# Performance work log

Measured on AMD Instinct MI355X. Metric: run time of the kernel, lower is better.

The kernel has to match this reference:

```python
import jax, jax.numpy as jnp
import numpy as np

B, C, H, W = 8, 192, 128, 128
E, HID, TOP_K = 4, 384, 2


def setup_inputs() -> dict:
    key = jax.random.key(0)
    ks = jax.random.split(key, 5)
    sn = lambda k, sh, sc: jax.random.normal(k, sh, jnp.float32) * sc
    return {
        "x": jax.random.normal(ks[0], (B, C, H, W), jnp.float32),
        "router_w": sn(ks[1], (E, C), C ** -0.5),
        "router_b": jnp.zeros((E,), jnp.float32),
        "fc1_w": sn(ks[2], (E, HID, C), C ** -0.5),
        "fc1_b": jnp.zeros((E, HID), jnp.float32),
        "fc2_w": sn(ks[3], (E, C, HID), HID ** -0.5),
        "fc2_b": jnp.zeros((E, C), jnp.float32),
        "scale": jnp.array([0.1], jnp.float32),
    }


def reference(x, router_w, router_b, fc1_w, fc1_b, fc2_w, fc2_b, scale):
    b, c, h, w = x.shape
    e = router_w.shape[0]
    # (B,C,H,W) -> (B, N, C) tokens
    tokens = jnp.transpose(x, (0, 2, 3, 1)).reshape(b, h * w, c)
    logits = tokens @ router_w.T + router_b            # (B,N,E)
    topv, topi = jax.lax.top_k(logits, TOP_K)          # (B,N,K)
    wts = jax.nn.softmax(topv, axis=-1)                # (B,N,K)
    # per-expert combine weight: sum_k wts_k * [topi_k == e]  -> (B,N,E)
    gates = jnp.sum(jax.nn.one_hot(topi, e, dtype=tokens.dtype) * wts[..., None], axis=-2)
    out = jnp.zeros_like(tokens)
    for ei in range(e):  # small fixed expert count
        hid = jax.nn.gelu(tokens @ fc1_w[ei].T + fc1_b[ei], approximate=False)
        y_e = hid @ fc2_w[ei].T + fc2_b[ei]
        out = out + gates[..., ei:ei + 1] * y_e
    out = jnp.transpose(out.reshape(b, h, w, c), (0, 3, 1, 2))
    return x + scale[0] * out
```

## Files before the change

### kernel.cpp

```cpp
#include <hip/hip_runtime.h>
#include <stdint.h>

typedef __attribute__((ext_vector_type(4))) float f32x4;
typedef unsigned long long u64;
typedef __attribute__((ext_vector_type(2))) u64 u64x2;

#define CC   192
#define NN   16384
#define EE   4
#define HIDD 384

#define OFF_H0   12800u
#define OFF_H1   25600u
#define OFF_PART 12800
#define OFF_GATE 38400
#define LDS_SZ   39424
#define ROWS     200u

__device__ __forceinline__ uint32_t fp8b(float f){
  uint32_t u = __builtin_bit_cast(uint32_t, f);
  uint32_t s = (u >> 24) & 0x80u;
  float af = fminf(__builtin_fabsf(f), 448.0f);
  if (af < 0.015625f) return s;
  uint32_t v = __builtin_bit_cast(uint32_t, af);
  v += 0x7FFFFu + ((v >> 20) & 1u);
  uint32_t e = (v >> 23) - 120u;
  return s | (e << 3) | ((v >> 20) & 7u);
}
#if __has_builtin(__builtin_amdgcn_cvt_pk_fp8_f32)
__device__ __forceinline__ uint32_t fp8x4(float a, float b, float c, float d){
  int v = __builtin_amdgcn_cvt_pk_fp8_f32(a, b, 0, false);
  v = __builtin_amdgcn_cvt_pk_fp8_f32(c, d, v, true);
  return (uint32_t)v;
}
#else
__device__ __forceinline__ uint32_t fp8x4(float a, float b, float c, float d){
  return fp8b(a) | (fp8b(b) << 8) | (fp8b(c) << 16) | (fp8b(d) << 24);
}
#endif
__device__ __forceinline__ float gelu_f(float v){
  float e = __builtin_amdgcn_exp2f(v * -2.4554669f);
  return v * __builtin_amdgcn_rcpf(1.0f + e);
}
__device__ __forceinline__ f32x4 mfma8(u64 a, u64 b, f32x4 c){
  asm("v_mfma_f32_16x16x32_fp8_fp8 %0, %1, %2, %0" : "+v"(c) : "v"(a), "v"(b));
  return c;
}

#define WAITV(n) do{ asm volatile("s_waitcnt vmcnt(" #n ")"); \
                     __builtin_amdgcn_sched_barrier(0); }while(0)
#define BARRIER() do{ __builtin_amdgcn_sched_barrier(0); \
                      asm volatile("s_waitcnt lgkmcnt(0)"); \
                      __builtin_amdgcn_s_barrier(); \
                      __builtin_amdgcn_sched_barrier(0); }while(0)

__device__ __forceinline__ void issue_w1(const uint8_t* a0, const uint8_t* a1,
                                         const uint8_t* a2, const float* bb,
                                         u64x2 (&w)[9], f32x4 (&bv)[3]){
  asm volatile(
    "global_load_dwordx4 %0, %[A0], off\n\t"
    "global_load_dwordx4 %1, %[A0], off offset:16\n\t"
    "global_load_dwordx4 %2, %[A0], off offset:32\n\t"
    "global_load_dwordx4 %3, %[A1], off\n\t"
    "global_load_dwordx4 %4, %[A1], off offset:16\n\t"
    "global_load_dwordx4 %5, %[A1], off offset:32\n\t"
    "global_load_dwordx4 %6, %[A2], off\n\t"
    "global_load_dwordx4 %7, %[A2], off offset:16\n\t"
    "global_load_dwordx4 %8, %[A2], off offset:32\n\t"
    "global_load_dwordx4 %9, %[B], off\n\t"
    "global_load_dwordx4 %10, %[B], off offset:64\n\t"
    "global_load_dwordx4 %11, %[B], off offset:128"
    : "=&v"(w[0]), "=&v"(w[1]), "=&v"(w[2]), "=&v"(w[3]), "=&v"(w[4]), "=&v"(w[5]),
      "=&v"(w[6]), "=&v"(w[7]), "=&v"(w[8]), "=&v"(bv[0]), "=&v"(bv[1]), "=&v"(bv[2])
    : [A0]"v"(a0), [A1]"v"(a1), [A2]"v"(a2), [B]"v"(bb));
}
__device__ __forceinline__ void issue_w2(const uint8_t* a0, const uint8_t* a1,
                                         const uint8_t* a2, u64x2 (&w)[9]){
  asm volatile(
    "global_load_dwordx4 %0, %[A0], off\n\t"
    "global_load_dwordx4 %1, %[A0], off offset:16\n\t"
    "global_load_dwordx4 %2, %[A0], off offset:32\n\t"
    "global_load_dwordx4 %3, %[A1], off\n\t"
    "global_load_dwordx4 %4, %[A1], off offset:16\n\t"
    "global_load_dwordx4 %5, %[A1], off offset:32\n\t"
    "global_load_dwordx4 %6, %[A2], off\n\t"
    "global_load_dwordx4 %7, %[A2], off offset:16\n\t"
    "global_load_dwordx4 %8, %[A2], off offset:32"
    : "=&v"(w[0]), "=&v"(w[1]), "=&v"(w[2]), "=&v"(w[3]), "=&v"(w[4]), "=&v"(w[5]),
      "=&v"(w[6]), "=&v"(w[7]), "=&v"(w[8])
    : [A0]"v"(a0), [A1]"v"(a1), [A2]"v"(a2));
}

extern "C" __global__ void kconv(const float* __restrict__ w1, const float* __restrict__ w2,
                                 uint8_t* __restrict__ w1f8, uint8_t* __restrict__ w2f8){
  int i = blockIdx.x * 256 + threadIdx.x;
  {
    int row = i / 192, k = i % 192;
    int o = k >> 3, kk = o >> 2, lg = o & 3, bi = k & 7;
    w1f8[(size_t)row * 192 + lg * 48 + kk * 8 + bi] = (uint8_t)fp8b(w1[i]);
  }
  {
    int row = i / 384, k = i % 384;
    int o = k >> 3, kk = o >> 2, lg = o & 3, bi = k & 7;
    w2f8[(size_t)row * 384 + lg * 96 + kk * 8 + bi] = (uint8_t)fp8b(w2[i]);
  }
}

__global__ __launch_bounds__(256)
__attribute__((amdgpu_waves_per_eu(2, 2)))
void kmoe(const float* __restrict__ x, const float* __restrict__ rw,
          const float* __restrict__ rb, const uint8_t* __restrict__ w1f8,
          const float* __restrict__ b1, const uint8_t* __restrict__ w2f8,
          const float* __restrict__ b2, const float* __restrict__ scp,
          float* __restrict__ out)
{
  __shared__ __align__(16) unsigned char S[LDS_SZ];
  const int tid  = threadIdx.x;
  const int lane = tid & 63;
  const int wv   = tid >> 6;
  const int lq   = lane & 15;
  const int lg   = lane >> 4;
  const int tile = blockIdx.x;
  const int b    = tile >> 8;
  const int n0   = (tile & 255) << 6;
  const float* xb = x + (size_t)b * CC * NN;

  {
    const int t = lane;
    const uint32_t rowbase = (uint32_t)t * ROWS;
    float a0 = 0.f, a1 = 0.f, a2 = 0.f, a3 = 0.f;
    #pragma unroll
    for (int jj = 0; jj < 6; ++jj){
      float v[8];
      #pragma unroll
      for (int j = 0; j < 8; ++j){
        const int c = wv * 48 + jj * 8 + j;
        v[j] = xb[(size_t)c * NN + n0 + t];
        a0 = __builtin_fmaf(v[j], rw[c],          a0);
        a1 = __builtin_fmaf(v[j], rw[CC + c],     a1);
        a2 = __builtin_fmaf(v[j], rw[2 * CC + c], a2);
        a3 = __builtin_fmaf(v[j], rw[3 * CC + c], a3);
      }
      uint2 p;
      p.x = fp8x4(v[0], v[1], v[2], v[3]);
      p.y = fp8x4(v[4], v[5], v[6], v[7]);
      *(uint2*)(S + rowbase + (uint32_t)(wv * 48 + jj * 8)) = p;
    }
    float* pl = (float*)(S + OFF_PART);
    pl[(wv * 4 + 0) * 64 + t] = a0;
    pl[(wv * 4 + 1) * 64 + t] = a1;
    pl[(wv * 4 + 2) * 64 + t] = a2;
    pl[(wv * 4 + 3) * 64 + t] = a3;
  }
  __syncthreads();

  if (tid < 64){
    const int t = tid;
    const float* pl = (const float*)(S + OFF_PART);
    float l0 = rb[0], l1 = rb[1], l2 = rb[2], l3 = rb[3];
    #pragma unroll
    for (int cg = 0; cg < 4; ++cg){
      l0 += pl[(cg * 4 + 0) * 64 + t];
      l1 += pl[(cg * 4 + 1) * 64 + t];
      l2 += pl[(cg * 4 + 2) * 64 + t];
      l3 += pl[(cg * 4 + 3) * 64 + t];
    }
    int i1 = 0; float v1 = l0;
    if (l1 > v1){ v1 = l1; i1 = 1; }
    if (l2 > v1){ v1 = l2; i1 = 2; }
    if (l3 > v1){ v1 = l3; i1 = 3; }
    float v2 = -3.0e38f; int i2 = 0;
    if (i1 != 0){ v2 = l0; i2 = 0; }
    if (i1 != 1 && l1 > v2){ v2 = l1; i2 = 1; }
    if (i1 != 2 && l2 > v2){ v2 = l2; i2 = 2; }
    if (i1 != 3 && l3 > v2){ v2 = l3; i2 = 3; }
    const float ex = __expf(v2 - v1);
    const float ga = 1.0f / (1.0f + ex);
    const float gb = ex * ga;
    float* glw = (float*)(S + OFF_GATE);
    glw[t * 4 + 0] = (i1 == 0) ? ga : ((i2 == 0) ? gb : 0.0f);
    glw[t * 4 + 1] = (i1 == 1) ? ga : ((i2 == 1) ? gb : 0.0f);
    glw[t * 4 + 2] = (i1 == 2) ? ga : ((i2 == 2) ? gb : 0.0f);
    glw[t * 4 + 3] = (i1 == 3) ? ga : ((i2 == 3) ? gb : 0.0f);
  }
  __syncthreads();

  const float* gl = (const float*)(S + OFF_GATE);
  uint32_t rowb[4];
  #pragma unroll
  for (int np = 0; np < 4; ++np) rowb[np] = (uint32_t)(16 * np + lq) * ROWS;

  const uint8_t* w1l = w1f8 + (size_t)(wv * 48 + lq) * 192 + lg * 48;
  const uint8_t* w2l = w2f8 + (size_t)(wv * 48 + lq) * 384 + lg * 96;
  const float*   b1l = b1 + wv * 48 + 4 * lg;

  u64x2 W1[9], W2[9];
  f32x4 BV[3];
  f32x4 oacc[3][4];
  #pragma unroll
  for (int m = 0; m < 3; ++m)
    #pragma unroll
    for (int np = 0; np < 4; ++np)
      oacc[m][np] = (f32x4){0.f, 0.f, 0.f, 0.f};

#define ISSUE_W1(p) issue_w1(w1l + (size_t)(p) * 36864, \
                             w1l + (size_t)(p) * 36864 + 16 * 192, \
                             w1l + (size_t)(p) * 36864 + 32 * 192, \
                             b1l + (p) * 192, W1, BV)
#define ISSUE_W2(e, ch) issue_w2(w2l + (size_t)(e) * 73728 + (ch) * 48, \
                                 w2l + (size_t)(e) * 73728 + (ch) * 48 + 16 * 384, \
                                 w2l + (size_t)(e) * 73728 + (ch) * 48 + 32 * 384, W2)

#define G1_COMP(hacc) do{ \
    _Pragma("unroll") \
    for (int m = 0; m < 3; ++m) \
      _Pragma("unroll") \
      for (int np = 0; np < 4; ++np) hacc[m][np] = BV[m]; \
    __builtin_amdgcn_s_setprio(1); \
    _Pragma("unroll") \
    for (int kk = 0; kk < 6; ++kk){ \
      u64 xk[4]; \
      _Pragma("unroll") \
      for (int np = 0; np < 4; ++np) \
        xk[np] = *(const u64*)(S + rowb[np] + (uint32_t)(kk * 32 + lg * 8)); \
      _Pragma("unroll") \
      for (int np = 0; np < 4; ++np) \
        _Pragma("unroll") \
        for (int m = 0; m < 3; ++m){ \
          const u64 a = (kk & 1) ? W1[m * 3 + (kk >> 1)].y : W1[m * 3 + (kk >> 1)].x; \
          hacc[m][np] = mfma8(a, xk[np], hacc[m][np]); \
        } \
    } \
    __builtin_amdgcn_s_setprio(0); }while(0)

#define G2_COMP(hb) do{ \
    __builtin_amdgcn_s_setprio(1); \
    _Pragma("unroll") \
    for (int kk = 0; kk < 6; ++kk){ \
      u64 hf[4]; \
      _Pragma("unroll") \
      for (int np = 0; np < 4; ++np) \
        hf[np] = *(const u64*)(S + (hb) + rowb[np] + (uint32_t)(kk * 32 + lg * 8)); \
      _Pragma("unroll") \
      for (int np = 0; np < 4; ++np) \
        _Pragma("unroll") \
        for (int m = 0; m < 3; ++m){ \
          const u64 a = (kk & 1) ? W2[m * 3 + (kk >> 1)].y : W2[m * 3 + (kk >> 1)].x; \
          oacc[m][np] = mfma8(a, hf[np], oacc[m][np]); \
        } \
    } \
    __builtin_amdgcn_s_setprio(0); }while(0)

#define GELU_ST(hb, e, hacc) do{ \
    _Pragma("unroll") \
    for (int np = 0; np < 4; ++np){ \
      const float g = gl[(16 * np + lq) * 4 + (e)]; \
      _Pragma("unroll") \
      for (int m = 0; m < 3; ++m){ \
        const uint32_t colb = (uint32_t)(48 * wv + 16 * m + 4 * lg); \
        *(uint32_t*)(S + (hb) + rowb[np] + colb) = \
          fp8x4(gelu_f(hacc[m][np][0]) * g, gelu_f(hacc[m][np][1]) * g, \
                gelu_f(hacc[m][np][2]) * g, gelu_f(hacc[m][np][3]) * g); \
      } \
    } }while(0)

  {
    ISSUE_W1(0);
    ISSUE_W2(0, 0);
    WAITV(9);
    f32x4 hacc[3][4];
    G1_COMP(hacc);
    GELU_ST(OFF_H0, 0, hacc);
    ISSUE_W1(1);
  }
  BARRIER();

  #pragma unroll 1
  for (int i = 0; i < 7; ++i){
    const uint32_t hb_r = (i & 1) ? OFF_H1 : OFF_H0;
    const uint32_t hb_w = (i & 1) ? OFF_H0 : OFF_H1;
    WAITV(12);
    G2_COMP(hb_r);
    {
      const int p = i + 1;
      ISSUE_W2(p >> 1, p & 1);
    }
    WAITV(9);
    f32x4 hacc[3][4];
    G1_COMP(hacc);
    GELU_ST(hb_w, (i + 1) >> 1, hacc);
    if (i < 6) ISSUE_W1(i + 2);
    BARRIER();
  }

  WAITV(0);
  G2_COMP(OFF_H1);

  {
    const float sc = scp[0];
    f32x4 g4v[4];
    #pragma unroll
    for (int np = 0; np < 4; ++np)
      g4v[np] = *(const f32x4*)(S + OFF_GATE + (16 * np + lq) * 16);
    const size_t obase = (size_t)b * CC * NN + n0;
    #pragma unroll
    for (int m = 0; m < 3; ++m){
      const int f0 = 48 * wv + 16 * m + 4 * lg;
      f32x4 b2q[4];
      #pragma unroll
      for (int e = 0; e < 4; ++e)
        b2q[e] = *(const f32x4*)(b2 + e * CC + f0);
      #pragma unroll
      for (int np = 0; np < 4; ++np){
        const int tok = 16 * np + lq;
        #pragma unroll
        for (int r = 0; r < 4; ++r){
          const float bt = __builtin_fmaf(g4v[np][0], b2q[0][r],
                            __builtin_fmaf(g4v[np][1], b2q[1][r],
                             __builtin_fmaf(g4v[np][2], b2q[2][r],
                                            g4v[np][3] * b2q[3][r])));
          const size_t off = obase + (size_t)(f0 + r) * NN + tok;
          out[off] = __builtin_fmaf(sc, oacc[m][np][r] + bt, x[off]);
        }
      }
    }
  }
#undef ISSUE_W1
#undef ISSUE_W2
#undef G1_COMP
#undef G2_COMP
#undef GELU_ST
}

extern "C" void kernel_launch(void* const* d_in, const int* in_sizes, int n_in,
                              void* d_out, int out_size, void* d_ws, size_t ws_size,
                              hipStream_t stream){
  const float* x  = (const float*)d_in[0];
  const float* rw = (const float*)d_in[1];
  const float* rb = (const float*)d_in[2];
  const float* w1 = (const float*)d_in[3];
  const float* b1 = (const float*)d_in[4];
  const float* w2 = (const float*)d_in[5];
  const float* b2 = (const float*)d_in[6];
  const float* sc = (const float*)d_in[7];
  float* out = (float*)d_out;
  uint8_t* w1f8 = (uint8_t*)d_ws;
  uint8_t* w2f8 = w1f8 + 294912;

  hipLaunchKernelGGL(kconv, dim3(1152), dim3(256), 0, stream, w1, w2, w1f8, w2f8);
  hipLaunchKernelGGL(kmoe,  dim3(2048), dim3(256), 0, stream,
                     x, rw, rb, w1f8, b1, w2f8, b2, sc, out);
}
```

Baseline: 166.3 us.

## Route tokens per expert via LDS lists to skip unselected token-expert pairs

Builds per-expert token lists in LDS with ballot/popcount after the router, so each expert's FC1/FC2 MFMA work runs only over groups of 16 tokens that actually selected it. This replaces the dense compute of all four experts for every token. Partial outputs are scattered into a new fp32 LDS accumulation buffer, and the final epilogue reads from it to do the coalesced residual write. In exchange, LDS use roughly doubles, which can lower occupancy, and the change adds extra barriers, gather indirection and LDS read-modify-write traffic.

```diff
diff --git a/kernel.cpp b/kernel.cpp
--- a/kernel.cpp
+++ b/kernel.cpp
@@ -10,12 +10,16 @@
 #define EE   4
 #define HIDD 384
 
-#define OFF_H0   12800u
-#define OFF_H1   25600u
-#define OFF_PART 12800
-#define OFF_GATE 38400
-#define LDS_SZ   39424
-#define ROWS     200u
+#define OFF_X    0u
+#define OFF_HID  12800u
+#define OFF_PART 12800u
+#define OFF_OUT  25600u
+#define OFF_GATE 76560u
+#define OFF_LIST 77584u
+#define OFF_CNT  78608u
+#define LDS_SZ   78640
+#define XROWB    200u
+#define OROWB    784u
 
 __device__ __forceinline__ uint32_t fp8b(float f){
   uint32_t u = __builtin_bit_cast(uint32_t, f);
@@ -127,7 +131,7 @@
 
   {
     const int t = lane;
-    const uint32_t rowbase = (uint32_t)t * ROWS;
+    const uint32_t rowbase = (uint32_t)t * XROWB;
     float a0 = 0.f, a1 = 0.f, a2 = 0.f, a3 = 0.f;
     #pragma unroll
     for (int jj = 0; jj < 6; ++jj){
@@ -182,13 +186,30 @@
     glw[t * 4 + 1] = (i1 == 1) ? ga : ((i2 == 1) ? gb : 0.0f);
     glw[t * 4 + 2] = (i1 == 2) ? ga : ((i2 == 2) ? gb : 0.0f);
     glw[t * 4 + 3] = (i1 == 3) ? ga : ((i2 == 3) ? gb : 0.0f);
+    uint32_t* lst = (uint32_t*)(S + OFF_LIST);
+    uint32_t* cw  = (uint32_t*)(S + OFF_CNT);
+    #pragma unroll
+    for (int e = 0; e < 4; ++e){
+      const bool mine = (i1 == e) || (i2 == e);
+      const u64 msk = __ballot(mine);
+      const int cnt = __popcll(msk);
+      const int ng  = (cnt + 15) >> 4;
+      if (mine){
+        const int slot = (int)__popcll(msk & ((1ull << t) - 1ull));
+        lst[e * 64 + slot] = (uint32_t)t;
+      }
+      if (t >= cnt && t < ng * 16) lst[e * 64 + t] = 0u;
+      if (t == 0){ cw[e] = (uint32_t)ng; cw[4 + e] = (uint32_t)cnt; }
+    }
   }
   __syncthreads();
 
   const float* gl = (const float*)(S + OFF_GATE);
-  uint32_t rowb[4];
+  const uint32_t* lst = (const uint32_t*)(S + OFF_LIST);
+  const int* cw = (const int*)(S + OFF_CNT);
+  uint32_t rowh[4];
   #pragma unroll
-  for (int np = 0; np < 4; ++np) rowb[np] = (uint32_t)(16 * np + lq) * ROWS;
+  for (int np = 0; np < 4; ++np) rowh[np] = OFF_HID + (uint32_t)(16 * np + lq) * XROWB;
 
   const uint8_t* w1l = w1f8 + (size_t)(wv * 48 + lq) * 192 + lg * 48;
   const uint8_t* w2l = w2f8 + (size_t)(wv * 48 + lq) * 384 + lg * 96;
@@ -210,126 +231,173 @@
 #define ISSUE_W2(e, ch) issue_w2(w2l + (size_t)(e) * 73728 + (ch) * 48, \
                                  w2l + (size_t)(e) * 73728 + (ch) * 48 + 16 * 384, \
                                  w2l + (size_t)(e) * 73728 + (ch) * 48 + 32 * 384, W2)
-
-#define G1_COMP(hacc) do{ \
+#define LOAD_TOK(tk, e) do{ \
+    _Pragma("unroll") \
+    for (int np = 0; np < 4; ++np) tk[np] = lst[(e) * 64 + np * 16 + lq]; }while(0)
+
+#define G1_NP(np, tk, hacc) do{ \
+    const uint32_t xrow = OFF_X + tk[np] * XROWB; \
+    _Pragma("unroll") \
+    for (int kk = 0; kk < 6; ++kk){ \
+      const u64 xk = *(const u64*)(S + xrow + (uint32_t)(kk * 32 + lg * 8)); \
+      _Pragma("unroll") \
+      for (int m = 0; m < 3; ++m){ \
+        const u64 a = (kk & 1) ? W1[m * 3 + (kk >> 1)].y : W1[m * 3 + (kk >> 1)].x; \
+        hacc[m][np] = mfma8(a, xk, hacc[m][np]); \
+      } \
+    } }while(0)
+#define G1_COMP(ng, tk, hacc) do{ \
     _Pragma("unroll") \
     for (int m = 0; m < 3; ++m) \
       _Pragma("unroll") \
       for (int np = 0; np < 4; ++np) hacc[m][np] = BV[m]; \
     __builtin_amdgcn_s_setprio(1); \
+    if (0 < (ng)) G1_NP(0, tk, hacc); \
+    if (1 < (ng)) G1_NP(1, tk, hacc); \
+    if (2 < (ng)) G1_NP(2, tk, hacc); \
+    if (3 < (ng)) G1_NP(3, tk, hacc); \
+    __builtin_amdgcn_s_setprio(0); }while(0)
+
+#define G2_NP(np) do{ \
     _Pragma("unroll") \
     for (int kk = 0; kk < 6; ++kk){ \
-      u64 xk[4]; \
+      const u64 hf = *(const u64*)(S + rowh[np] + (uint32_t)(kk * 32 + lg * 8)); \
       _Pragma("unroll") \
-      for (int np = 0; np < 4; ++np) \
-        xk[np] = *(const u64*)(S + rowb[np] + (uint32_t)(kk * 32 + lg * 8)); \
-      _Pragma("unroll") \
-      for (int np = 0; np < 4; ++np) \
+      for (int m = 0; m < 3; ++m){ \
+        const u64 a = (kk & 1) ? W2[m * 3 + (kk >> 1)].y : W2[m * 3 + (kk >> 1)].x; \
+        oacc[m][np] = mfma8(a, hf, oacc[m][np]); \
+      } \
+    } }while(0)
+#define G2_COMP(ng) do{ \
+    __builtin_amdgcn_s_setprio(1); \
+    if (0 < (ng)) G2_NP(0); \
+    if (1 < (ng)) G2_NP(1); \
+    if (2 < (ng)) G2_NP(2); \
+    if (3 < (ng)) G2_NP(3); \
+    __builtin_amdgcn_s_setprio(0); }while(0)
+
+#define GELU_ST(e, ng, ct, tk, hacc) do{ \
+    _Pragma("unroll") \
+    for (int np = 0; np < 4; ++np){ \
+      if (np < (ng)){ \
+        const float g = (np * 16 + lq < (ct)) ? gl[tk[np] * 4 + (e)] : 0.0f; \
         _Pragma("unroll") \
         for (int m = 0; m < 3; ++m){ \
-          const u64 a = (kk & 1) ? W1[m * 3 + (kk >> 1)].y : W1[m * 3 + (kk >> 1)].x; \
-          hacc[m][np] = mfma8(a, xk[np], hacc[m][np]); \
+          *(uint32_t*)(S + rowh[np] + (uint32_t)(48 * wv + 16 * m + 4 * lg)) = \
+            fp8x4(gelu_f(hacc[m][np][0]) * g, gelu_f(hacc[m][np][1]) * g, \
+                  gelu_f(hacc[m][np][2]) * g, gelu_f(hacc[m][np][3]) * g); \
         } \
-    } \
-    __builtin_amdgcn_s_setprio(0); }while(0)
-
-#define G2_COMP(hb) do{ \
-    __builtin_amdgcn_s_setprio(1); \
-    _Pragma("unroll") \
-    for (int kk = 0; kk < 6; ++kk){ \
-      u64 hf[4]; \
-      _Pragma("unroll") \
-      for (int np = 0; np < 4; ++np) \
-        hf[np] = *(const u64*)(S + (hb) + rowb[np] + (uint32_t)(kk * 32 + lg * 8)); \
-      _Pragma("unroll") \
-      for (int np = 0; np < 4; ++np) \
+      } \
+    } }while(0)
+
+#define SCATTER(e, ng, ct, tk) do{ \
+    _Pragma("unroll") \
+    for (int np = 0; np < 4; ++np){ \
+      if (np < (ng)){ \
+        const uint32_t srow = (np * 16 + lq < (ct)) ? tk[np] : 64u; \
         _Pragma("unroll") \
         for (int m = 0; m < 3; ++m){ \
-          const u64 a = (kk & 1) ? W2[m * 3 + (kk >> 1)].y : W2[m * 3 + (kk >> 1)].x; \
-          oacc[m][np] = mfma8(a, hf[np], oacc[m][np]); \
+          float* p = (float*)(S + OFF_OUT + srow * OROWB \
+                              + (uint32_t)((48 * wv + 16 * m + 4 * lg) * 4)); \
+          f32x4 c = *(const f32x4*)p; \
+          c += oacc[m][np]; \
+          *(f32x4*)p = c; \
         } \
-    } \
-    __builtin_amdgcn_s_setprio(0); }while(0)
-
-#define GELU_ST(hb, e, hacc) do{ \
-    _Pragma("unroll") \
-    for (int np = 0; np < 4; ++np){ \
-      const float g = gl[(16 * np + lq) * 4 + (e)]; \
+      } \
       _Pragma("unroll") \
-      for (int m = 0; m < 3; ++m){ \
-        const uint32_t colb = (uint32_t)(48 * wv + 16 * m + 4 * lg); \
-        *(uint32_t*)(S + (hb) + rowb[np] + colb) = \
-          fp8x4(gelu_f(hacc[m][np][0]) * g, gelu_f(hacc[m][np][1]) * g, \
-                gelu_f(hacc[m][np][2]) * g, gelu_f(hacc[m][np][3]) * g); \
-      } \
+      for (int m = 0; m < 3; ++m) oacc[m][np] = (f32x4){0.f, 0.f, 0.f, 0.f}; \
     } }while(0)
 
-  {
-    ISSUE_W1(0);
-    ISSUE_W2(0, 0);
+  ISSUE_W1(0);
+  ISSUE_W2(0, 0);
+  {
+    f32x4* oz = (f32x4*)(S + OFF_OUT);
+    for (int i = tid; i < 65 * 49; i += 256) oz[i] = (f32x4){0.f, 0.f, 0.f, 0.f};
+  }
+  {
+    const int ng = __builtin_amdgcn_readfirstlane(cw[0]);
+    const int ct = __builtin_amdgcn_readfirstlane(cw[4]);
+    uint32_t tk[4];
+    LOAD_TOK(tk, 0);
     WAITV(9);
     f32x4 hacc[3][4];
-    G1_COMP(hacc);
-    GELU_ST(OFF_H0, 0, hacc);
+    G1_COMP(ng, tk, hacc);
+    GELU_ST(0, ng, ct, tk, hacc);
     ISSUE_W1(1);
   }
   BARRIER();
 
   #pragma unroll 1
   for (int i = 0; i < 7; ++i){
-    const uint32_t hb_r = (i & 1) ? OFF_H1 : OFF_H0;
-    const uint32_t hb_w = (i & 1) ? OFF_H0 : OFF_H1;
+    const int e2 = i >> 1;
+    const int p1 = i + 1, e1 = p1 >> 1, ch1 = p1 & 1;
     WAITV(12);
-    G2_COMP(hb_r);
     {
-      const int p = i + 1;
-      ISSUE_W2(p >> 1, p & 1);
-    }
+      const int ng2 = __builtin_amdgcn_readfirstlane(cw[e2]);
+      G2_COMP(ng2);
+      if (i & 1){
+        const int ct2 = __builtin_amdgcn_readfirstlane(cw[4 + e2]);
+        uint32_t tk2[4];
+        LOAD_TOK(tk2, e2);
+        SCATTER(e2, ng2, ct2, tk2);
+      }
+    }
+    ISSUE_W2(e1, ch1);
     WAITV(9);
-    f32x4 hacc[3][4];
-    G1_COMP(hacc);
-    GELU_ST(hb_w, (i + 1) >> 1, hacc);
+    {
+      const int ng1 = __builtin_amdgcn_readfirstlane(cw[e1]);
+      const int ct1 = __builtin_amdgcn_readfirstlane(cw[4 + e1]);
+      uint32_t tk1[4];
+      LOAD_TOK(tk1, e1);
+      f32x4 hacc[3][4];
+      G1_COMP(ng1, tk1, hacc);
+      BARRIER();
+      GELU_ST(e1, ng1, ct1, tk1, hacc);
+    }
     if (i < 6) ISSUE_W1(i + 2);
     BARRIER();
   }
 
   WAITV(0);
-  G2_COMP(OFF_H1);
-
-  {
+  {
+    const int ng = __builtin_amdgcn_readfirstlane(cw[3]);
+    const int ct = __builtin_amdgcn_readfirstlane(cw[4 + 3]);
+    G2_COMP(ng);
+    uint32_t tk[4];
+    LOAD_TOK(tk, 3);
+    SCATTER(3, ng, ct, tk);
+  }
+  BARRIER();
+
+  {
+    const int t = lane;
     const float sc = scp[0];
-    f32x4 g4v[4];
+    const f32x4 g4 = *(const f32x4*)(S + OFF_GATE + t * 16);
+    const float* xbt = xb + n0 + t;
+    float* ob = out + (size_t)b * CC * NN + n0 + t;
     #pragma unroll
-    for (int np = 0; np < 4; ++np)
-      g4v[np] = *(const f32x4*)(S + OFF_GATE + (16 * np + lq) * 16);
-    const size_t obase = (size_t)b * CC * NN + n0;
-    #pragma unroll
-    for (int m = 0; m < 3; ++m){
-      const int f0 = 48 * wv + 16 * m + 4 * lg;
-      f32x4 b2q[4];
+    for (int j = 0; j < 12; ++j){
+      const int c0 = wv * 48 + j * 4;
+      const f32x4 v = *(const f32x4*)(S + OFF_OUT + (uint32_t)t * OROWB + c0 * 4);
       #pragma unroll
-      for (int e = 0; e < 4; ++e)
-        b2q[e] = *(const f32x4*)(b2 + e * CC + f0);
-      #pragma unroll
-      for (int np = 0; np < 4; ++np){
-        const int tok = 16 * np + lq;
-        #pragma unroll
-        for (int r = 0; r < 4; ++r){
-          const float bt = __builtin_fmaf(g4v[np][0], b2q[0][r],
-                            __builtin_fmaf(g4v[np][1], b2q[1][r],
-                             __builtin_fmaf(g4v[np][2], b2q[2][r],
-                                            g4v[np][3] * b2q[3][r])));
-          const size_t off = obase + (size_t)(f0 + r) * NN + tok;
-          out[off] = __builtin_fmaf(sc, oacc[m][np][r] + bt, x[off]);
-        }
+      for (int r = 0; r < 4; ++r){
+        const int c = c0 + r;
+        const float bt = __builtin_fmaf(g4[0], b2[c],
+                          __builtin_fmaf(g4[1], b2[CC + c],
+                           __builtin_fmaf(g4[2], b2[2 * CC + c], g4[3] * b2[3 * CC + c])));
+        ob[(size_t)c * NN] = __builtin_fmaf(sc, v[r] + bt, xbt[(size_t)c * NN]);
       }
     }
   }
 #undef ISSUE_W1
 #undef ISSUE_W2
+#undef LOAD_TOK
+#undef G1_NP
 #undef G1_COMP
+#undef G2_NP
 #undef G2_COMP
 #undef GELU_ST
+#undef SCATTER
 }
 
 extern "C" void kernel_launch(void* const* d_in, const int* in_sizes, int n_in,
```

Measured after the change: 190.1 us. +14.3%, slower.
